# Performance work log

Hardware: AMD Instinct MI355X
Metric: run time of the kernel (lower is better)

Reference implementation:

```python
import jax, jax.numpy as jnp
import numpy as np

NEG_SLOPE = 0.2  # negative_slope of LeakyReLU in GATConv
N_NODES = 50000
N_EDGES = 800000
R = 2
IN_DIM = 128
HID = 32
HEADS = 4
OUT = 32


def setup_inputs() -> dict:
    key = jax.random.key(0)
    ks = jax.random.split(key, 12)
    s = 0.1  # keep pre-activations tame
    x = jax.random.normal(ks[0], (N_NODES, IN_DIM), dtype=jnp.float32)
    W1 = jax.random.normal(ks[1], (R, IN_DIM, HEADS * HID), dtype=jnp.float32) * s
    al1 = jax.random.normal(ks[2], (R, HEADS, HID), dtype=jnp.float32) * s
    ar1 = jax.random.normal(ks[3], (R, HEADS, HID), dtype=jnp.float32) * s
    b1 = jax.random.normal(ks[4], (R, HEADS * HID), dtype=jnp.float32) * s
    W2 = jax.random.normal(ks[5], (R, HEADS * HID, HEADS * OUT), dtype=jnp.float32) * s
    al2 = jax.random.normal(ks[6], (R, HEADS, OUT), dtype=jnp.float32) * s
    ar2 = jax.random.normal(ks[7], (R, HEADS, OUT), dtype=jnp.float32) * s
    b2 = jax.random.normal(ks[8], (R, HEADS * OUT), dtype=jnp.float32) * s
    edges = jax.random.randint(ks[9], (R, 2, N_EDGES), 0, N_NODES, dtype=jnp.int32)
    return {"x": x, "W1": W1, "al1": al1, "ar1": ar1, "b1": b1,
            "W2": W2, "al2": al2, "ar2": ar2, "b2": b2, "edges": edges}


def _gat_rel(h, W, al, ar, src, dst, n):
    """Single-relation GATConv aggregation (no bias/residual/activation)."""
    H, D = al.shape
    feat = (h @ W).reshape(n, H, D)                   # [N,H,D]
    el = jnp.einsum('nhd,hd->nh', feat, al)           # [N,H]
    er = jnp.einsum('nhd,hd->nh', feat, ar)
    e = el[src] + er[dst]                             # [E,H]
    e = jnp.where(e > 0, e, NEG_SLOPE * e)            # LeakyReLU
    # edge softmax over incoming edges of each dst node (numerically stable)
    m = jax.ops.segment_max(e, dst, num_segments=n)
    ex = jnp.exp(e - m[dst])
    denom = jax.ops.segment_sum(ex, dst, num_segments=n)
    alpha = ex / jnp.maximum(denom[dst], 1e-9)        # [E,H]
    msg = alpha[:, :, None] * feat[src]               # [E,H,D]
    return jax.ops.segment_sum(msg, dst, num_segments=n)  # [N,H,D]


def reference(x, W1, al1, ar1, b1, W2, al2, ar2, b2, edges):
    n = x.shape[0]
    r_count = edges.shape[0]
    H1, D1 = al1.shape[1:]
    # --- layer 1: per-relation GATConv (bias + elu inside), sum across relations
    acc = jnp.zeros((n, H1, D1), dtype=x.dtype)
    for r in range(r_count):
        src, dst = edges[r, 0], edges[r, 1]
        o = _gat_rel(x, W1[r], al1[r], ar1[r], src, dst, n)
        acc = acc + jax.nn.elu(o + b1[r].reshape(1, H1, D1))
    h = acc.reshape(n, H1 * D1)                       # flatten heads
    # --- layer 2: residual (identity, since in == heads*out), bias, no activation
    H2, D2 = al2.shape[1:]
    res = h.reshape(n, H2, D2)
    acc2 = jnp.zeros((n, H2, D2), dtype=x.dtype)
    for r in range(r_count):
        src, dst = edges[r, 0], edges[r, 1]
        o = _gat_rel(h, W2[r], al2[r], ar2[r], src, dst, n)
        acc2 = acc2 + o + res + b2[r].reshape(1, H2, D2)
    return acc2.mean(axis=1)                          # mean over heads -> [N, OUT]
```

## Files before the change

### kernel.cpp

```cpp
#include <hip/hip_runtime.h>
#include <math.h>

#define HEADS 4
#define DIM 32
#define FDIM 128
#define EPB 8192
#define BPBSH 8
#define WB 16

typedef __attribute__((ext_vector_type(8))) short short8;
typedef __attribute__((ext_vector_type(16))) float float16;

__device__ __forceinline__ unsigned short f2bf(float x) {
  unsigned u = __float_as_uint(x);
  u += 0x7FFFu + ((u >> 16) & 1);
  return (unsigned short)(u >> 16);
}

__global__ __launch_bounds__(256) void binA_kernel(const int* __restrict__ edges,
    int* __restrict__ cntA, const float* __restrict__ W1, const float* __restrict__ W2,
    unsigned short* __restrict__ WT, int E, int BA, int BAp, int R) {
  int r = blockIdx.y, blk = blockIdx.x, t = threadIdx.x;
  if (blk >= BA) {
    int wb = blk - BA;
    int base = wb * (32768 / WB);
#pragma unroll
    for (int j = 0; j < 32768 / WB; j += 256) {
      int idx = base + j + t;
      int layer = idx >> 14;
      int rem = idx & 16383;
      int n = rem >> 7, k = rem & 127;
      const float* W = layer ? (W2 + (size_t)r * FDIM * FDIM)
                             : (W1 + (size_t)r * FDIM * FDIM);
      WT[((size_t)(layer * R + r) << 14) + rem] = f2bf(W[k * FDIM + n]);
    }
    return;
  }
  __shared__ int hist[256];
  hist[t] = 0;
  __syncthreads();
  const int* dst = edges + (size_t)r * 2 * E + E;
  int base = blk * EPB;
#pragma unroll
  for (int j = 0; j < EPB / 256; ++j) {
    int e = base + t + j * 256;
    if (e < E) atomicAdd(&hist[dst[e] >> BPBSH], 1);
  }
  __syncthreads();
  cntA[((size_t)r * 256 + t) * BAp + blk] = hist[t];
}

__global__ __launch_bounds__(256) void scanA_kernel(int* __restrict__ cntA,
    int* __restrict__ bucketBase, int E, int NB, int BA, int BAp) {
  __shared__ int stot[256];
  int r = blockIdx.x, b = threadIdx.x;
  int* row = cntA + ((size_t)r * 256 + b) * BAp;
  int tot = 0;
  if (b < NB)
    for (int blk = 0; blk < BA; ++blk) tot += row[blk];
  stot[b] = tot;
  __syncthreads();
  for (int ofs = 1; ofs < 256; ofs <<= 1) {
    int u = (b >= ofs) ? stot[b - ofs] : 0;
    __syncthreads();
    stot[b] += u;
    __syncthreads();
  }
  int excl = stot[b] - tot;
  if (b < NB) bucketBase[r * 257 + b] = excl;
  if (b == 0) bucketBase[r * 257 + NB] = E;
  if (b < NB) {
    int run = excl;
    for (int blk = 0; blk < BA; ++blk) {
      int c = row[blk];
      row[blk] = run;
      run += c;
    }
  }
}

__global__ __launch_bounds__(256) void scatterA_kernel(const int* __restrict__ edges,
    const int* __restrict__ cntA, unsigned* __restrict__ binned, int E, int BA, int BAp) {
  __shared__ int cur[256];
  int r = blockIdx.y, blk = blockIdx.x, t = threadIdx.x;
  cur[t] = cntA[((size_t)r * 256 + t) * BAp + blk];
  __syncthreads();
  const int* srcp = edges + (size_t)r * 2 * E;
  const int* dstp = srcp + E;
  unsigned* bout = binned + (size_t)r * E;
  int base = blk * EPB;
#pragma unroll
  for (int j = 0; j < EPB / 256; ++j) {
    int e = base + t + j * 256;
    if (e < E) {
      int d = dstp[e], s = srcp[e];
      int pos = atomicAdd(&cur[d >> BPBSH], 1);
      bout[pos] = ((unsigned)d << 16) | (unsigned)s;
    }
  }
}

__global__ __launch_bounds__(256) void passB_kernel(const unsigned* __restrict__ binned,
    const int* __restrict__ bucketBase, int* __restrict__ csr, int* __restrict__ indptr,
    int E, int N, int NB) {
  __shared__ int cnt[256];
  __shared__ int off[256];
  __shared__ int cur[256];
  int r = blockIdx.y, b = blockIdx.x, t = threadIdx.x;
  int beg = bucketBase[r * 257 + b];
  int end = bucketBase[r * 257 + b + 1];
  cnt[t] = 0;
  __syncthreads();
  const unsigned* bin = binned + (size_t)r * E;
  for (int i = beg + t; i < end; i += 256)
    atomicAdd(&cnt[(bin[i] >> 16) & 255], 1);
  __syncthreads();
  for (int ofs = 1; ofs < 256; ofs <<= 1) {
    int u = (t >= ofs) ? cnt[t - ofs] : 0;
    __syncthreads();
    cnt[t] += u;
    __syncthreads();
  }
  int ex = beg + ((t > 0) ? cnt[t - 1] : 0);
  off[t] = ex;
  cur[t] = ex;
  __syncthreads();
  int node = b * 256 + t;
  if (node < N) indptr[(size_t)r * (N + 1) + node] = off[t];
  if (b == NB - 1 && t == 0) indptr[(size_t)r * (N + 1) + N] = E;
  int* csr_r = csr + (size_t)r * E;
  for (int i = beg + t; i < end; i += 256) {
    unsigned p = bin[i];
    int rank = atomicAdd(&cur[(p >> 16) & 255], 1);
    csr_r[rank] = (int)(p & 0xFFFFu);
  }
}

__global__ __launch_bounds__(256) void mm_kernel(const float* __restrict__ A,
    const unsigned short* __restrict__ WTl, const float* __restrict__ al_all,
    const float* __restrict__ ar_all, unsigned short* __restrict__ featb_all,
    float* __restrict__ el_all, float* __restrict__ er_all, int N) {
  __shared__ unsigned short sA[128 * 136];
  __shared__ float sAl[FDIM], sAr[FDIM];
  int r = blockIdx.y;
  const unsigned short* WT = WTl + (size_t)r * FDIM * FDIM;
  int row0 = blockIdx.x * 128;
  int t = threadIdx.x;
  if (t < FDIM) {
    sAl[t] = al_all[r * FDIM + t];
    sAr[t] = ar_all[r * FDIM + t];
  }
#pragma unroll
  for (int it = 0; it < 16; ++it) {
    int idx = t * 4 + it * 1024;
    int row = idx >> 7, k = idx & 127;
    int grow = row0 + row;
    float4 v = make_float4(0.f, 0.f, 0.f, 0.f);
    if (grow < N) v = *(const float4*)(A + (size_t)grow * FDIM + k);
    unsigned short* p = sA + row * 136 + k;
    p[0] = f2bf(v.x); p[1] = f2bf(v.y); p[2] = f2bf(v.z); p[3] = f2bf(v.w);
  }
  __syncthreads();
  int lane = t & 63, w = t >> 6;
  int m = lane & 31, q = lane >> 5;
  float16 acc[4] = {0.f, 0.f, 0.f, 0.f};
#pragma unroll
  for (int kc = 0; kc < 8; ++kc) {
    int ko = kc * 16 + q * 8;
    short8 a = *(const short8*)(sA + (w * 32 + m) * 136 + ko);
#pragma unroll
    for (int nt = 0; nt < 4; ++nt) {
      short8 bb = *(const short8*)(WT + (size_t)(nt * 32 + m) * FDIM + ko);
      acc[nt] = __builtin_amdgcn_mfma_f32_32x32x16_bf16(a, bb, acc[nt], 0, 0, 0);
    }
  }
  __syncthreads();
#pragma unroll
  for (int nt = 0; nt < 4; ++nt) {
#pragma unroll
    for (int reg = 0; reg < 16; ++reg) {
      int rr = (reg & 3) + 8 * (reg >> 2) + 4 * q;
      sA[(w * 32 + rr) * 136 + nt * 32 + m] = f2bf(acc[nt][reg]);
    }
  }
  __syncthreads();
  unsigned short* fb = featb_all + (size_t)r * N * FDIM;
#pragma unroll
  for (int it = 0; it < 8; ++it) {
    int idx = (t + it * 256) * 8;
    int row = idx >> 7, k = idx & 127;
    int grow = row0 + row;
    if (grow < N)
      *(uint4*)(fb + (size_t)grow * FDIM + k) = *(const uint4*)(sA + row * 136 + k);
  }
  int rowc = t >> 1, grow = row0 + rowc;
  if (grow < N) {
    float* elr = el_all + (size_t)r * N * 4;
    float* err_ = er_all + (size_t)r * N * 4;
#pragma unroll
    for (int hh = 0; hh < 2; ++hh) {
      int hd = (t & 1) * 2 + hh;
      const uint4* rp4 = (const uint4*)(sA + rowc * 136 + hd * DIM);
      const float4* alp = (const float4*)(sAl + hd * DIM);
      const float4* arp = (const float4*)(sAr + hd * DIM);
      float sl = 0.f, sr = 0.f;
#pragma unroll
      for (int gq = 0; gq < 4; ++gq) {
        uint4 u = rp4[gq];
        float4 a0 = alp[2 * gq], a1 = alp[2 * gq + 1];
        float4 r0 = arp[2 * gq], r1 = arp[2 * gq + 1];
        unsigned uv[4] = {u.x, u.y, u.z, u.w};
        float fv[8];
#pragma unroll
        for (int j = 0; j < 4; ++j) {
          fv[2 * j] = __uint_as_float(uv[j] << 16);
          fv[2 * j + 1] = __uint_as_float(uv[j] & 0xFFFF0000u);
        }
        sl = fmaf(fv[0], a0.x, sl); sr = fmaf(fv[0], r0.x, sr);
        sl = fmaf(fv[1], a0.y, sl); sr = fmaf(fv[1], r0.y, sr);
        sl = fmaf(fv[2], a0.z, sl); sr = fmaf(fv[2], r0.z, sr);
        sl = fmaf(fv[3], a0.w, sl); sr = fmaf(fv[3], r0.w, sr);
        sl = fmaf(fv[4], a1.x, sl); sr = fmaf(fv[4], r1.x, sr);
        sl = fmaf(fv[5], a1.y, sl); sr = fmaf(fv[5], r1.y, sr);
        sl = fmaf(fv[6], a1.z, sl); sr = fmaf(fv[6], r1.z, sr);
        sl = fmaf(fv[7], a1.w, sl); sr = fmaf(fv[7], r1.w, sr);
      }
      elr[(size_t)grow * 4 + hd] = sl;
      err_[(size_t)grow * 4 + hd] = sr;
    }
  }
}

__device__ __forceinline__ void acc16(float (&a)[16], uint4 u0, uint4 u1, float p) {
  unsigned uu[8] = {u0.x, u0.y, u0.z, u0.w, u1.x, u1.y, u1.z, u1.w};
#pragma unroll
  for (int j = 0; j < 8; ++j) {
    float f0 = __uint_as_float(uu[j] << 16);
    float f1 = __uint_as_float(uu[j] & 0xFFFF0000u);
    a[2 * j]     = fmaf(p, f0, a[2 * j]);
    a[2 * j + 1] = fmaf(p, f1, a[2 * j + 1]);
  }
}

__global__ __launch_bounds__(256) void agg1_kernel(const unsigned short* __restrict__ featb,
    const float* __restrict__ el, const float* __restrict__ er,
    const int* __restrict__ indptr, const int* __restrict__ csr,
    const float* __restrict__ bias, float* __restrict__ hout, int N, int E, int R) {
  int t = blockIdx.x * 256 + threadIdx.x;
  int node = t >> 5;
  if (node >= N) return;
  int hd = t & 3, half = (t >> 2) & 1, rr = (t >> 3) & 1, sub = (t >> 4) & 1;
  float tot[16];
#pragma unroll
  for (int i = 0; i < 16; ++i) tot[i] = 0.f;
  for (int r = rr; r < R; r += 2) {
    const unsigned short* f = featb + (size_t)r * N * FDIM + hd * DIM + half * 16;
    const float* elr = el + (size_t)r * N * 4;
    const int* csr_r = csr + (size_t)r * E;
    const int* ip = indptr + (size_t)r * (N + 1);
    float er_h = er[(size_t)r * N * 4 + node * 4 + hd];
    int beg = ip[node], end = ip[node + 1];
    float l = 0.f, a[16];
#pragma unroll
    for (int i = 0; i < 16; ++i) a[i] = 0.f;
    int i = beg + sub;
    for (; i + 2 < end; i += 4) {
      int s0 = csr_r[i], s1 = csr_r[i + 2];
      const uint4* fp0 = (const uint4*)(f + (size_t)s0 * FDIM);
      const uint4* fp1 = (const uint4*)(f + (size_t)s1 * FDIM);
      float ee0 = elr[s0 * 4 + hd];
      float ee1 = elr[s1 * 4 + hd];
      uint4 u00 = fp0[0], u01 = fp0[1];
      uint4 u10 = fp1[0], u11 = fp1[1];
      ee0 += er_h; ee0 = ee0 > 0.f ? ee0 : 0.2f * ee0;
      ee1 += er_h; ee1 = ee1 > 0.f ? ee1 : 0.2f * ee1;
      float p0 = __expf(ee0), p1 = __expf(ee1);
      l += p0 + p1;
      acc16(a, u00, u01, p0);
      acc16(a, u10, u11, p1);
    }
    if (i < end) {
      int s = csr_r[i];
      const uint4* fp = (const uint4*)(f + (size_t)s * FDIM);
      float ee = elr[s * 4 + hd] + er_h;
      uint4 u0 = fp[0], u1 = fp[1];
      ee = ee > 0.f ? ee : 0.2f * ee;
      float p = __expf(ee);
      l += p;
      acc16(a, u0, u1, p);
    }
    l += __shfl_xor(l, 16);
#pragma unroll
    for (int k = 0; k < 16; ++k) a[k] += __shfl_xor(a[k], 16);
    float inv = (l > 0.f) ? 1.f / l : 0.f;
    const float4* b4 = (const float4*)(bias + r * FDIM + hd * DIM + half * 16);
#pragma unroll
    for (int g = 0; g < 4; ++g) {
      float4 bv = b4[g];
      float v0 = a[4 * g] * inv + bv.x;
      float v1 = a[4 * g + 1] * inv + bv.y;
      float v2 = a[4 * g + 2] * inv + bv.z;
      float v3 = a[4 * g + 3] * inv + bv.w;
      tot[4 * g]     += v0 > 0.f ? v0 : __expf(v0) - 1.f;
      tot[4 * g + 1] += v1 > 0.f ? v1 : __expf(v1) - 1.f;
      tot[4 * g + 2] += v2 > 0.f ? v2 : __expf(v2) - 1.f;
      tot[4 * g + 3] += v3 > 0.f ? v3 : __expf(v3) - 1.f;
    }
  }
#pragma unroll
  for (int k = 0; k < 16; ++k) tot[k] += __shfl_xor(tot[k], 8);
  if ((t & 24) == 0) {
    float4* hp = (float4*)(hout + (size_t)node * FDIM + hd * DIM + half * 16);
#pragma unroll
    for (int g = 0; g < 4; ++g)
      hp[g] = make_float4(tot[4 * g], tot[4 * g + 1], tot[4 * g + 2], tot[4 * g + 3]);
  }
}

__global__ __launch_bounds__(256) void agg2_kernel(const unsigned short* __restrict__ featb,
    const float* __restrict__ el, const float* __restrict__ er,
    const int* __restrict__ indptr, const int* __restrict__ csr,
    const float* __restrict__ bias, const float* __restrict__ hf,
    float* __restrict__ out, int N, int E, int R) {
  int t = blockIdx.x * 256 + threadIdx.x;
  int node = t >> 5;
  if (node >= N) return;
  int hd = t & 3, half = (t >> 2) & 1, rr = (t >> 3) & 1, sub = (t >> 4) & 1;
  float tot[16];
#pragma unroll
  for (int i = 0; i < 16; ++i) tot[i] = 0.f;
  for (int r = rr; r < R; r += 2) {
    const unsigned short* f = featb + (size_t)r * N * FDIM + hd * DIM + half * 16;
    const float* elr = el + (size_t)r * N * 4;
    const int* csr_r = csr + (size_t)r * E;
    const int* ip = indptr + (size_t)r * (N + 1);
    float er_h = er[(size_t)r * N * 4 + node * 4 + hd];
    int beg = ip[node], end = ip[node + 1];
    float l = 0.f, a[16];
#pragma unroll
    for (int i = 0; i < 16; ++i) a[i] = 0.f;
    int i = beg + sub;
    for (; i + 2 < end; i += 4) {
      int s0 = csr_r[i], s1 = csr_r[i + 2];
      const uint4* fp0 = (const uint4*)(f + (size_t)s0 * FDIM);
      const uint4* fp1 = (const uint4*)(f + (size_t)s1 * FDIM);
      float ee0 = elr[s0 * 4 + hd];
      float ee1 = elr[s1 * 4 + hd];
      uint4 u00 = fp0[0], u01 = fp0[1];
      uint4 u10 = fp1[0], u11 = fp1[1];
      ee0 += er_h; ee0 = ee0 > 0.f ? ee0 : 0.2f * ee0;
      ee1 += er_h; ee1 = ee1 > 0.f ? ee1 : 0.2f * ee1;
      float p0 = __expf(ee0), p1 = __expf(ee1);
      l += p0 + p1;
      acc16(a, u00, u01, p0);
      acc16(a, u10, u11, p1);
    }
    if (i < end) {
      int s = csr_r[i];
      const uint4* fp = (const uint4*)(f + (size_t)s * FDIM);
      float ee = elr[s * 4 + hd] + er_h;
      uint4 u0 = fp[0], u1 = fp[1];
      ee = ee > 0.f ? ee : 0.2f * ee;
      float p = __expf(ee);
      l += p;
      acc16(a, u0, u1, p);
    }
    l += __shfl_xor(l, 16);
#pragma unroll
    for (int k = 0; k < 16; ++k) a[k] += __shfl_xor(a[k], 16);
    float inv = (l > 0.f) ? 1.f / l : 0.f;
    const float4* b4 = (const float4*)(bias + r * FDIM + hd * DIM + half * 16);
#pragma unroll
    for (int g = 0; g < 4; ++g) {
      float4 bv = b4[g];
      tot[4 * g]     += a[4 * g] * inv + bv.x;
      tot[4 * g + 1] += a[4 * g + 1] * inv + bv.y;
      tot[4 * g + 2] += a[4 * g + 2] * inv + bv.z;
      tot[4 * g + 3] += a[4 * g + 3] * inv + bv.w;
    }
  }
#pragma unroll
  for (int k = 0; k < 16; ++k) tot[k] += __shfl_xor(tot[k], 8);
  {
    const float4* rv4 = (const float4*)(hf + (size_t)node * FDIM + hd * DIM + half * 16);
#pragma unroll
    for (int g = 0; g < 4; ++g) {
      float4 rv = rv4[g];
      tot[4 * g]     += R * rv.x;
      tot[4 * g + 1] += R * rv.y;
      tot[4 * g + 2] += R * rv.z;
      tot[4 * g + 3] += R * rv.w;
    }
  }
#pragma unroll
  for (int i = 0; i < 16; ++i) {
    float v = tot[i];
    v += __shfl_xor(v, 1);
    v += __shfl_xor(v, 2);
    tot[i] = v * 0.25f;
  }
  if ((t & 27) == 0) {
    float4* op = (float4*)(out + (size_t)node * 32 + half * 16);
#pragma unroll
    for (int g = 0; g < 4; ++g)
      op[g] = make_float4(tot[4 * g], tot[4 * g + 1], tot[4 * g + 2], tot[4 * g + 3]);
  }
}

extern "C" void kernel_launch(void* const* d_in, const int* in_sizes, int n_in,
                              void* d_out, int out_size, void* d_ws, size_t ws_size,
                              hipStream_t stream) {
  const float* x   = (const float*)d_in[0];
  const float* W1  = (const float*)d_in[1];
  const float* al1 = (const float*)d_in[2];
  const float* ar1 = (const float*)d_in[3];
  const float* b1  = (const float*)d_in[4];
  const float* W2  = (const float*)d_in[5];
  const float* al2 = (const float*)d_in[6];
  const float* ar2 = (const float*)d_in[7];
  const float* b2  = (const float*)d_in[8];
  const int* edges = (const int*)d_in[9];
  float* out = (float*)d_out;

  const int N = in_sizes[0] / FDIM;
  const int R = in_sizes[1] / (FDIM * FDIM);
  const int E = in_sizes[9] / (2 * R);
  const int BA = (E + EPB - 1) / EPB;
  const int BAp = (BA + 3) & ~3;
  const int NB = (N + 255) >> BPBSH;

  char* ws = (char*)d_ws;
  size_t off = 0;
  auto alloc = [&](size_t bytes) {
    char* p = ws + off;
    off += (bytes + 255) & ~(size_t)255;
    return p;
  };
  unsigned short* featb = (unsigned short*)alloc((size_t)R * N * FDIM * 2);
  unsigned short* WT    = (unsigned short*)alloc((size_t)2 * R * FDIM * FDIM * 2);
  float* el = (float*)alloc((size_t)R * N * 4 * 4);
  float* er = (float*)alloc((size_t)R * N * 4 * 4);
  float* h  = (float*)alloc((size_t)N * FDIM * 4);
  int* cntA = (int*)alloc((size_t)R * 256 * BAp * 4);
  int* bucketBase = (int*)alloc((size_t)R * 257 * 4);
  unsigned* binned = (unsigned*)alloc((size_t)R * E * 4);
  int* csr = (int*)alloc((size_t)R * E * 4);
  int* indptr = (int*)alloc((size_t)R * (N + 1) * 4);

  dim3 bgrid(BA + WB, R);
  binA_kernel<<<bgrid, 256, 0, stream>>>(edges, cntA, W1, W2, WT, E, BA, BAp, R);
  scanA_kernel<<<R, 256, 0, stream>>>(cntA, bucketBase, E, NB, BA, BAp);
  dim3 sgrid(BA, R);
  scatterA_kernel<<<sgrid, 256, 0, stream>>>(edges, cntA, binned, E, BA, BAp);
  dim3 pgrid(NB, R);
  passB_kernel<<<pgrid, 256, 0, stream>>>(binned, bucketBase, csr, indptr, E, N, NB);

  dim3 mmgrid((N + 127) / 128, R);
  int agrid = (N * 32 + 255) / 256;

  mm_kernel<<<mmgrid, 256, 0, stream>>>(x, WT, al1, ar1, featb, el, er, N);
  agg1_kernel<<<agrid, 256, 0, stream>>>(featb, el, er, indptr, csr, b1, h, N, E, R);

  mm_kernel<<<mmgrid, 256, 0, stream>>>(h, WT + (size_t)R * FDIM * FDIM, al2, ar2, featb, el, er, N);
  agg2_kernel<<<agrid, 256, 0, stream>>>(featb, el, er, indptr, csr, b2, h, out, N, E, R);
}
```

Measured before the change: 373.5 us.

## Slice aggregation by feature block across blocks, use 16-bit CSR and head-major logits

The aggregation kernels now map each block to one of 8 sixteen-wide feature slices for 128 nodes, with two lanes per node, instead of spreading one node's heads, halves and relations across 32 lanes. Concurrent blocks working on the same slice gather a narrower band of the feature table, which should improve cache locality. Source indices are stored as 16-bit values, and el/er are laid out head-major, to reduce gather bytes. Layer 2 writes per-slice partial results to a scratch buffer, and a new reduce kernel averages them over heads. This adds an extra kernel launch and buffer traffic, and the 16-bit CSR is only valid while node indices stay below 65536.

New measurement: 638.6 us. +71.0%, slower.

```diff
diff --git a/kernel.cpp b/kernel.cpp
--- a/kernel.cpp
+++ b/kernel.cpp
@@ -101,8 +101,8 @@
 }
 
 __global__ __launch_bounds__(256) void passB_kernel(const unsigned* __restrict__ binned,
-    const int* __restrict__ bucketBase, int* __restrict__ csr, int* __restrict__ indptr,
-    int E, int N, int NB) {
+    const int* __restrict__ bucketBase, unsigned short* __restrict__ csr,
+    int* __restrict__ indptr, int E, int N, int NB) {
   __shared__ int cnt[256];
   __shared__ int off[256];
   __shared__ int cur[256];
@@ -128,11 +128,11 @@
   int node = b * 256 + t;
   if (node < N) indptr[(size_t)r * (N + 1) + node] = off[t];
   if (b == NB - 1 && t == 0) indptr[(size_t)r * (N + 1) + N] = E;
-  int* csr_r = csr + (size_t)r * E;
+  unsigned short* csr_r = csr + (size_t)r * E;
   for (int i = beg + t; i < end; i += 256) {
     unsigned p = bin[i];
     int rank = atomicAdd(&cur[(p >> 16) & 255], 1);
-    csr_r[rank] = (int)(p & 0xFFFFu);
+    csr_r[rank] = (unsigned short)(p & 0xFFFFu);
   }
 }
 
@@ -195,8 +195,8 @@
   }
   int rowc = t >> 1, grow = row0 + rowc;
   if (grow < N) {
-    float* elr = el_all + (size_t)r * N * 4;
-    float* err_ = er_all + (size_t)r * N * 4;
+    float* elr = el_all + (size_t)r * 4 * N;
+    float* err_ = er_all + (size_t)r * 4 * N;
 #pragma unroll
     for (int hh = 0; hh < 2; ++hh) {
       int hd = (t & 1) * 2 + hh;
@@ -225,8 +225,8 @@
         sl = fmaf(fv[6], a1.z, sl); sr = fmaf(fv[6], r1.z, sr);
         sl = fmaf(fv[7], a1.w, sl); sr = fmaf(fv[7], r1.w, sr);
       }
-      elr[(size_t)grow * 4 + hd] = sl;
-      err_[(size_t)grow * 4 + hd] = sr;
+      elr[(size_t)hd * N + grow] = sl;
+      err_[(size_t)hd * N + grow] = sr;
     }
   }
 }
@@ -244,21 +244,24 @@
 
 __global__ __launch_bounds__(256) void agg1_kernel(const unsigned short* __restrict__ featb,
     const float* __restrict__ el, const float* __restrict__ er,
-    const int* __restrict__ indptr, const int* __restrict__ csr,
+    const int* __restrict__ indptr, const unsigned short* __restrict__ csr,
     const float* __restrict__ bias, float* __restrict__ hout, int N, int E, int R) {
-  int t = blockIdx.x * 256 + threadIdx.x;
-  int node = t >> 5;
+  int bix = blockIdx.x;
+  int slice = bix & 7, chunk = bix >> 3;
+  int node = chunk * 128 + (threadIdx.x >> 1);
+  int sub = threadIdx.x & 1;
   if (node >= N) return;
-  int hd = t & 3, half = (t >> 2) & 1, rr = (t >> 3) & 1, sub = (t >> 4) & 1;
+  int head = slice >> 1;
+  int doff = slice * 16;
   float tot[16];
 #pragma unroll
   for (int i = 0; i < 16; ++i) tot[i] = 0.f;
-  for (int r = rr; r < R; r += 2) {
-    const unsigned short* f = featb + (size_t)r * N * FDIM + hd * DIM + half * 16;
-    const float* elr = el + (size_t)r * N * 4;
-    const int* csr_r = csr + (size_t)r * E;
+  for (int r = 0; r < R; ++r) {
+    const unsigned short* f = featb + (size_t)r * N * FDIM + doff;
+    const float* el_h = el + ((size_t)r * 4 + head) * N;
+    const unsigned short* csr_r = csr + (size_t)r * E;
     const int* ip = indptr + (size_t)r * (N + 1);
-    float er_h = er[(size_t)r * N * 4 + node * 4 + hd];
+    float er_h = er[((size_t)r * 4 + head) * N + node];
     int beg = ip[node], end = ip[node + 1];
     float l = 0.f, a[16];
 #pragma unroll
@@ -268,8 +271,8 @@
       int s0 = csr_r[i], s1 = csr_r[i + 2];
       const uint4* fp0 = (const uint4*)(f + (size_t)s0 * FDIM);
       const uint4* fp1 = (const uint4*)(f + (size_t)s1 * FDIM);
-      float ee0 = elr[s0 * 4 + hd];
-      float ee1 = elr[s1 * 4 + hd];
+      float ee0 = el_h[s0];
+      float ee1 = el_h[s1];
       uint4 u00 = fp0[0], u01 = fp0[1];
       uint4 u10 = fp1[0], u11 = fp1[1];
       ee0 += er_h; ee0 = ee0 > 0.f ? ee0 : 0.2f * ee0;
@@ -282,18 +285,18 @@
     if (i < end) {
       int s = csr_r[i];
       const uint4* fp = (const uint4*)(f + (size_t)s * FDIM);
-      float ee = elr[s * 4 + hd] + er_h;
+      float ee = el_h[s] + er_h;
       uint4 u0 = fp[0], u1 = fp[1];
       ee = ee > 0.f ? ee : 0.2f * ee;
       float p = __expf(ee);
       l += p;
       acc16(a, u0, u1, p);
     }
-    l += __shfl_xor(l, 16);
-#pragma unroll
-    for (int k = 0; k < 16; ++k) a[k] += __shfl_xor(a[k], 16);
+    l += __shfl_xor(l, 1);
+#pragma unroll
+    for (int k = 0; k < 16; ++k) a[k] += __shfl_xor(a[k], 1);
     float inv = (l > 0.f) ? 1.f / l : 0.f;
-    const float4* b4 = (const float4*)(bias + r * FDIM + hd * DIM + half * 16);
+    const float4* b4 = (const float4*)(bias + r * FDIM + doff);
 #pragma unroll
     for (int g = 0; g < 4; ++g) {
       float4 bv = b4[g];
@@ -307,10 +310,8 @@
       tot[4 * g + 3] += v3 > 0.f ? v3 : __expf(v3) - 1.f;
     }
   }
-#pragma unroll
-  for (int k = 0; k < 16; ++k) tot[k] += __shfl_xor(tot[k], 8);
-  if ((t & 24) == 0) {
-    float4* hp = (float4*)(hout + (size_t)node * FDIM + hd * DIM + half * 16);
+  if (sub == 0) {
+    float4* hp = (float4*)(hout + (size_t)node * FDIM + doff);
 #pragma unroll
     for (int g = 0; g < 4; ++g)
       hp[g] = make_float4(tot[4 * g], tot[4 * g + 1], tot[4 * g + 2], tot[4 * g + 3]);
@@ -319,22 +320,25 @@
 
 __global__ __launch_bounds__(256) void agg2_kernel(const unsigned short* __restrict__ featb,
     const float* __restrict__ el, const float* __restrict__ er,
-    const int* __restrict__ indptr, const int* __restrict__ csr,
+    const int* __restrict__ indptr, const unsigned short* __restrict__ csr,
     const float* __restrict__ bias, const float* __restrict__ hf,
-    float* __restrict__ out, int N, int E, int R) {
-  int t = blockIdx.x * 256 + threadIdx.x;
-  int node = t >> 5;
+    float* __restrict__ P, int N, int E, int R) {
+  int bix = blockIdx.x;
+  int slice = bix & 7, chunk = bix >> 3;
+  int node = chunk * 128 + (threadIdx.x >> 1);
+  int sub = threadIdx.x & 1;
   if (node >= N) return;
-  int hd = t & 3, half = (t >> 2) & 1, rr = (t >> 3) & 1, sub = (t >> 4) & 1;
+  int head = slice >> 1;
+  int doff = slice * 16;
   float tot[16];
 #pragma unroll
   for (int i = 0; i < 16; ++i) tot[i] = 0.f;
-  for (int r = rr; r < R; r += 2) {
-    const unsigned short* f = featb + (size_t)r * N * FDIM + hd * DIM + half * 16;
-    const float* elr = el + (size_t)r * N * 4;
-    const int* csr_r = csr + (size_t)r * E;
+  for (int r = 0; r < R; ++r) {
+    const unsigned short* f = featb + (size_t)r * N * FDIM + doff;
+    const float* el_h = el + ((size_t)r * 4 + head) * N;
+    const unsigned short* csr_r = csr + (size_t)r * E;
     const int* ip = indptr + (size_t)r * (N + 1);
-    float er_h = er[(size_t)r * N * 4 + node * 4 + hd];
+    float er_h = er[((size_t)r * 4 + head) * N + node];
     int beg = ip[node], end = ip[node + 1];
     float l = 0.f, a[16];
 #pragma unroll
@@ -344,8 +348,8 @@
       int s0 = csr_r[i], s1 = csr_r[i + 2];
       const uint4* fp0 = (const uint4*)(f + (size_t)s0 * FDIM);
       const uint4* fp1 = (const uint4*)(f + (size_t)s1 * FDIM);
-      float ee0 = elr[s0 * 4 + hd];
-      float ee1 = elr[s1 * 4 + hd];
+      float ee0 = el_h[s0];
+      float ee1 = el_h[s1];
       uint4 u00 = fp0[0], u01 = fp0[1];
       uint4 u10 = fp1[0], u11 = fp1[1];
       ee0 += er_h; ee0 = ee0 > 0.f ? ee0 : 0.2f * ee0;
@@ -358,18 +362,18 @@
     if (i < end) {
       int s = csr_r[i];
       const uint4* fp = (const uint4*)(f + (size_t)s * FDIM);
-      float ee = elr[s * 4 + hd] + er_h;
+      float ee = el_h[s] + er_h;
       uint4 u0 = fp[0], u1 = fp[1];
       ee = ee > 0.f ? ee : 0.2f * ee;
       float p = __expf(ee);
       l += p;
       acc16(a, u0, u1, p);
     }
-    l += __shfl_xor(l, 16);
-#pragma unroll
-    for (int k = 0; k < 16; ++k) a[k] += __shfl_xor(a[k], 16);
+    l += __shfl_xor(l, 1);
+#pragma unroll
+    for (int k = 0; k < 16; ++k) a[k] += __shfl_xor(a[k], 1);
     float inv = (l > 0.f) ? 1.f / l : 0.f;
-    const float4* b4 = (const float4*)(bias + r * FDIM + hd * DIM + half * 16);
+    const float4* b4 = (const float4*)(bias + r * FDIM + doff);
 #pragma unroll
     for (int g = 0; g < 4; ++g) {
       float4 bv = b4[g];
@@ -379,10 +383,8 @@
       tot[4 * g + 3] += a[4 * g + 3] * inv + bv.w;
     }
   }
-#pragma unroll
-  for (int k = 0; k < 16; ++k) tot[k] += __shfl_xor(tot[k], 8);
   {
-    const float4* rv4 = (const float4*)(hf + (size_t)node * FDIM + hd * DIM + half * 16);
+    const float4* rv4 = (const float4*)(hf + (size_t)node * FDIM + doff);
 #pragma unroll
     for (int g = 0; g < 4; ++g) {
       float4 rv = rv4[g];
@@ -392,19 +394,24 @@
       tot[4 * g + 3] += R * rv.w;
     }
   }
-#pragma unroll
-  for (int i = 0; i < 16; ++i) {
-    float v = tot[i];
-    v += __shfl_xor(v, 1);
-    v += __shfl_xor(v, 2);
-    tot[i] = v * 0.25f;
-  }
-  if ((t & 27) == 0) {
-    float4* op = (float4*)(out + (size_t)node * 32 + half * 16);
+  if (sub == 0) {
+    float4* pp = (float4*)(P + (size_t)node * 128 + doff);
 #pragma unroll
     for (int g = 0; g < 4; ++g)
-      op[g] = make_float4(tot[4 * g], tot[4 * g + 1], tot[4 * g + 2], tot[4 * g + 3]);
-  }
+      pp[g] = make_float4(tot[4 * g], tot[4 * g + 1], tot[4 * g + 2], tot[4 * g + 3]);
+  }
+}
+
+__global__ __launch_bounds__(256) void reduce2_kernel(const float* __restrict__ P,
+    float* __restrict__ out, int N) {
+  int t = blockIdx.x * 256 + threadIdx.x;
+  int n = t >> 5, d = t & 31;
+  if (n >= N) return;
+  int dh = d >> 4, j = d & 15;
+  const float* p = P + (size_t)n * 128;
+  float v = p[(0 * 2 + dh) * 16 + j] + p[(1 * 2 + dh) * 16 + j] +
+            p[(2 * 2 + dh) * 16 + j] + p[(3 * 2 + dh) * 16 + j];
+  out[(size_t)n * 32 + d] = 0.25f * v;
 }
 
 extern "C" void kernel_launch(void* const* d_in, const int* in_sizes, int n_in,
@@ -441,10 +448,11 @@
   float* el = (float*)alloc((size_t)R * N * 4 * 4);
   float* er = (float*)alloc((size_t)R * N * 4 * 4);
   float* h  = (float*)alloc((size_t)N * FDIM * 4);
+  float* P  = (float*)alloc((size_t)N * FDIM * 4);
   int* cntA = (int*)alloc((size_t)R * 256 * BAp * 4);
   int* bucketBase = (int*)alloc((size_t)R * 257 * 4);
   unsigned* binned = (unsigned*)alloc((size_t)R * E * 4);
-  int* csr = (int*)alloc((size_t)R * E * 4);
+  unsigned short* csr = (unsigned short*)alloc((size_t)R * E * 2);
   int* indptr = (int*)alloc((size_t)R * (N + 1) * 4);
 
   dim3 bgrid(BA + WB, R);
@@ -456,11 +464,13 @@
   passB_kernel<<<pgrid, 256, 0, stream>>>(binned, bucketBase, csr, indptr, E, N, NB);
 
   dim3 mmgrid((N + 127) / 128, R);
-  int agrid = (N * 32 + 255) / 256;
+  int agrid = ((N + 127) / 128) * 8;
+  int rgrid = (N * 32 + 255) / 256;
 
   mm_kernel<<<mmgrid, 256, 0, stream>>>(x, WT, al1, ar1, featb, el, er, N);
   agg1_kernel<<<agrid, 256, 0, stream>>>(featb, el, er, indptr, csr, b1, h, N, E, R);
 
   mm_kernel<<<mmgrid, 256, 0, stream>>>(h, WT + (size_t)R * FDIM * FDIM, al2, ar2, featb, el, er, N);
-  agg2_kernel<<<agrid, 256, 0, stream>>>(featb, el, er, indptr, csr, b2, h, out, N, E, R);
-}
+  agg2_kernel<<<agrid, 256, 0, stream>>>(featb, el, er, indptr, csr, b2, h, P, N, E, R);
+  reduce2_kernel<<<rgrid, 256, 0, stream>>>(P, out, N);
+}
```
